# Optimization experiments

Hardware: AMD Instinct MI355X
Metric: run time of the kernel (lower is better)

The kernel has to match this reference:

```python
import jax, jax.numpy as jnp
import numpy as np

N, E, IN_DIM, H, D = 50000, 800000, 256, 4, 128
ALPHA = 0.2  # TF leaky_relu default


def setup_inputs() -> dict:
    key = jax.random.key(0)
    ks = jax.random.split(key, 8)
    s = 0.05  # glorot-like small init to keep exp() stable
    return {
        'features': jax.random.normal(ks[0], (N, IN_DIM), jnp.float32),
        'adj_indices': jax.random.randint(ks[1], (E, 2), 0, N, dtype=jnp.int64),
        'adj_values': jax.random.uniform(ks[2], (E,), jnp.float32),
        'W_trans': jax.random.normal(ks[3], (H, IN_DIM, D), jnp.float32) * s,
        'w_ftx': jax.random.normal(ks[4], (H, D, 1), jnp.float32) * s,
        'w_fty': jax.random.normal(ks[5], (H, D, 1), jnp.float32) * s,
        'w_view': jax.random.normal(ks[6], (H, 2 * D, 1), jnp.float32) * s,
        'bias': jnp.zeros((H, D), jnp.float32),
    }


def _seg_softmax(vals, seg, n):
    # tf.sparse_softmax: softmax over the explicit entries of each row
    m = jax.ops.segment_max(vals, seg, num_segments=n)
    m = jnp.where(jnp.isfinite(m), m, 0.0)  # rows with no edges
    e = jnp.exp(vals - m[seg])
    s = jax.ops.segment_sum(e, seg, num_segments=n)
    return e / s[seg]


def _forward(features, adj_indices, adj_values, W_trans, w_ftx, w_fty, w_view, bias):
    src = adj_indices[:, 0]
    dst = adj_indices[:, 1]
    n = features.shape[0]
    heads = []
    for h in range(W_trans.shape[0]):  # small fixed head count
        ft = features @ W_trans[h]  # [N, D]
        # tf.nn.l2_normalize(axis=1)
        ftn = ft * jax.lax.rsqrt(jnp.maximum(jnp.sum(ft * ft, axis=1, keepdims=True), 1e-12))
        # sim view: cosine similarity on edges
        sim_vals = jnp.sum(ftn[src] * ftn[dst], axis=1)  # [E]
        # nn view: GAT-style logits, leaky_relu, sparse softmax over rows
        ftx = (ft @ w_ftx[h])[:, 0]  # [N]
        fty = (ft @ w_fty[h])[:, 0]  # [N]
        nn_vals = _seg_softmax(jax.nn.leaky_relu(ftx[src] + fty[dst], ALPHA), src, n)
        # view representations: self + (click, sim, nn) each re-softmaxed then aggregated
        view_reprs = [ft]
        for vals in (adj_values, sim_vals, nn_vals):
            p = _seg_softmax(vals, src, n)  # [E]
            view_reprs.append(jax.ops.segment_sum(p[:, None] * ft[dst], src, num_segments=n))
        # learned view mixing: leaky_relu(concat(ft, repr) @ w_view), softmax(exp(.))
        va = [jax.nn.leaky_relu((jnp.concatenate([ft, vr], axis=1) @ w_view[h])[:, 0], ALPHA)
              for vr in view_reprs]
        coefs = jax.nn.softmax(jnp.exp(jnp.stack(va, axis=1)), axis=1)  # [N, 4]
        out = sum(vr * coefs[:, i:i + 1] for i, vr in enumerate(view_reprs)) + bias[h]
        heads.append(jax.nn.elu(out))
    return jnp.concatenate(heads, axis=-1)  # [N, H*D]


def reference(features, adj_indices, adj_values, W_trans, w_ftx, w_fty, w_view, bias):
    return _forward(features, adj_indices, adj_values, W_trans, w_ftx, w_fty, w_view, bias)
```

## Files before the change

kernel.cpp:

```cpp
#include <hip/hip_runtime.h>
#include <math.h>

#define LALPHA 0.2f

using bf16x8 = __attribute__((ext_vector_type(8))) short;
using f32x4 = __attribute__((ext_vector_type(4))) float;
using f32x2 = __attribute__((ext_vector_type(2))) float;

__device__ __forceinline__ float wave_sum(float v) {
#pragma unroll
  for (int off = 32; off > 0; off >>= 1) v += __shfl_xor(v, off);
  return v;
}
__device__ __forceinline__ float grp_sum(float v) {
#pragma unroll
  for (int off = 8; off > 0; off >>= 1) v += __shfl_xor(v, off);
  return v;
}
__device__ __forceinline__ float grp_max(float v) {
#pragma unroll
  for (int off = 8; off > 0; off >>= 1) v = fmaxf(v, __shfl_xor(v, off));
  return v;
}
__device__ __forceinline__ float lrelu(float x) { return x >= 0.f ? x : LALPHA * x; }

__device__ __forceinline__ f32x2 bfp2(unsigned int u) {
  f32x2 r;
  r[0] = __uint_as_float(u << 16);
  r[1] = __uint_as_float(u & 0xffff0000u);
  return r;
}
__device__ __forceinline__ unsigned short f2bf(float x) {
  unsigned int b = __float_as_uint(x);
  return (unsigned short)((b + 0x7fffu + ((b >> 16) & 1u)) >> 16);
}
__device__ __forceinline__ unsigned int cvtpk(float lo, float hi) {
  unsigned int r;
  asm("v_cvt_pk_bf16_f32 %0, %1, %2" : "=v"(r) : "v"(lo), "v"(hi));
  return r;
}

__global__ void hist_kernel(const int* __restrict__ adj, int* __restrict__ deg, int E) {
  for (int e = blockIdx.x * blockDim.x + threadIdx.x; e < E; e += gridDim.x * blockDim.x)
    atomicAdd(&deg[adj[2 * e]], 1);
}

__global__ __launch_bounds__(1024) void scan_a(const int* __restrict__ deg,
                                               int* __restrict__ row_ptr,
                                               int* __restrict__ tilesum, int n) {
  __shared__ int sm[1024];
  int tid = threadIdx.x;
  int idx = blockIdx.x * 1024 + tid;
  int v = (idx < n) ? deg[idx] : 0;
  sm[tid] = v;
  __syncthreads();
  for (int off = 1; off < 1024; off <<= 1) {
    int t = (tid >= off) ? sm[tid - off] : 0;
    __syncthreads();
    sm[tid] += t;
    __syncthreads();
  }
  if (idx < n) row_ptr[idx] = sm[tid] - v;
  if (tid == 1023) tilesum[blockIdx.x] = sm[1023];
}

__global__ __launch_bounds__(1024) void scan_b(int* __restrict__ tilesum, int ntiles) {
  __shared__ int sm[1024];
  int tid = threadIdx.x;
  int v = (tid < ntiles) ? tilesum[tid] : 0;
  sm[tid] = v;
  __syncthreads();
  for (int off = 1; off < 1024; off <<= 1) {
    int t = (tid >= off) ? sm[tid - off] : 0;
    __syncthreads();
    sm[tid] += t;
    __syncthreads();
  }
  if (tid < ntiles) tilesum[tid] = sm[tid] - v;
  if (tid == ntiles - 1) tilesum[ntiles] = sm[tid];
}

__global__ __launch_bounds__(1024) void scan_c(int* __restrict__ row_ptr,
                                               const int* __restrict__ tilesum, int n,
                                               int ntiles) {
  int idx = blockIdx.x * 1024 + threadIdx.x;
  if (idx < n) row_ptr[idx] += tilesum[blockIdx.x];
  if (idx == 0) row_ptr[n] = tilesum[ntiles];
}

__global__ void scatter_kernel(const int* __restrict__ adj, const float* __restrict__ av,
                               const int* __restrict__ row_ptr, int* __restrict__ cursor,
                               int2* __restrict__ csr_ew, int E) {
  for (int e = blockIdx.x * blockDim.x + threadIdx.x; e < E; e += gridDim.x * blockDim.x) {
    int s = adj[2 * e], d = adj[2 * e + 1];
    int pos = row_ptr[s] + atomicAdd(&cursor[s], 1);
    csr_ew[pos] = make_int2(d, __float_as_int(av[e]));
  }
}

__global__ void transw_kernel(const float* __restrict__ W, unsigned short* __restrict__ WT) {
  int idx = blockIdx.x * 256 + threadIdx.x;
  int d = idx & 127;
  int k = (idx >> 7) & 255;
  int h = idx >> 15;
  WT[((size_t)h * 128 + d) * 256 + k] = f2bf(W[idx]);
}

__global__ __launch_bounds__(256) void gemm_mfma(
    const float* __restrict__ A, const unsigned short* __restrict__ WT,
    unsigned short* __restrict__ ft, const float* __restrict__ w_ftx,
    const float* __restrict__ w_fty, float* __restrict__ rnorm, float* __restrict__ ftx,
    float* __restrict__ fty, int N, int H) {
  __shared__ unsigned short tile[4][32][136];
  const int K = 256;
  int h = blockIdx.x;
  int w = threadIdx.x >> 6;
  int r0 = blockIdx.y * 128 + w * 32;
  int lane = threadIdx.x & 63;
  int lr = lane & 15, lg = lane >> 4;
  int ra0 = min(r0 + lr, N - 1);
  int ra1 = min(r0 + 16 + lr, N - 1);
  const float* pa0 = A + (size_t)ra0 * K + lg * 8;
  const float* pa1 = A + (size_t)ra1 * K + lg * 8;
  const unsigned short* pb = WT + ((size_t)h * 128 + lr) * K + lg * 8;
  size_t st = (size_t)H * 128;

  f32x4 acc[2][8] = {};
  for (int k0 = 0; k0 < K; k0 += 32) {
    union {
      bf16x8 v;
      unsigned int u[4];
    } a0, a1;
    float4 f0 = *(const float4*)(pa0 + k0);
    float4 f1 = *(const float4*)(pa0 + k0 + 4);
    a0.u[0] = cvtpk(f0.x, f0.y);
    a0.u[1] = cvtpk(f0.z, f0.w);
    a0.u[2] = cvtpk(f1.x, f1.y);
    a0.u[3] = cvtpk(f1.z, f1.w);
    float4 g0 = *(const float4*)(pa1 + k0);
    float4 g1 = *(const float4*)(pa1 + k0 + 4);
    a1.u[0] = cvtpk(g0.x, g0.y);
    a1.u[1] = cvtpk(g0.z, g0.w);
    a1.u[2] = cvtpk(g1.x, g1.y);
    a1.u[3] = cvtpk(g1.z, g1.w);
    bf16x8 b[8];
#pragma unroll
    for (int cb = 0; cb < 8; ++cb) b[cb] = *(const bf16x8*)(pb + (size_t)cb * 16 * K + k0);
#pragma unroll
    for (int cb = 0; cb < 8; ++cb) {
      acc[0][cb] = __builtin_amdgcn_mfma_f32_16x16x32_bf16(a0.v, b[cb], acc[0][cb], 0, 0, 0);
      acc[1][cb] = __builtin_amdgcn_mfma_f32_16x16x32_bf16(a1.v, b[cb], acc[1][cb], 0, 0, 0);
    }
  }
#pragma unroll
  for (int i = 0; i < 2; ++i) {
#pragma unroll
    for (int cb = 0; cb < 8; ++cb) {
      int rbase = i * 16 + lg * 4;
      int col = cb * 16 + lr;
      unsigned int u01 = cvtpk(acc[i][cb][0], acc[i][cb][1]);
      unsigned int u23 = cvtpk(acc[i][cb][2], acc[i][cb][3]);
      tile[w][rbase + 0][col] = (unsigned short)u01;
      tile[w][rbase + 1][col] = (unsigned short)(u01 >> 16);
      tile[w][rbase + 2][col] = (unsigned short)u23;
      tile[w][rbase + 3][col] = (unsigned short)(u23 >> 16);
    }
  }
#pragma unroll
  for (int rr = 0; rr < 8; ++rr) {
    int row = rr * 4 + lg;
    int nb = r0 + row;
    if (nb < N) {
      *(uint4*)&ft[(size_t)nb * st + (size_t)h * 128 + lr * 8] =
          *(const uint4*)&tile[w][row][lr * 8];
    }
  }
  {
    int row = lane >> 1;
    int ch = lane & 1;
    int nb = r0 + row;
    const float* wx = w_ftx + (size_t)h * 128 + ch * 64;
    const float* wy = w_fty + (size_t)h * 128 + ch * 64;
    float ss = 0.f, sx = 0.f, sy = 0.f;
#pragma unroll
    for (int c8 = 0; c8 < 8; ++c8) {
      const unsigned int* tp = (const unsigned int*)&tile[w][row][ch * 64 + c8 * 8];
      f32x2 f0 = bfp2(tp[0]), f1 = bfp2(tp[1]), f2 = bfp2(tp[2]), f3 = bfp2(tp[3]);
      float4 x0 = *(const float4*)(wx + c8 * 8);
      float4 x1 = *(const float4*)(wx + c8 * 8 + 4);
      float4 y0 = *(const float4*)(wy + c8 * 8);
      float4 y1 = *(const float4*)(wy + c8 * 8 + 4);
      ss += f0[0] * f0[0] + f0[1] * f0[1] + f1[0] * f1[0] + f1[1] * f1[1] +
            f2[0] * f2[0] + f2[1] * f2[1] + f3[0] * f3[0] + f3[1] * f3[1];
      sx += f0[0] * x0.x + f0[1] * x0.y + f1[0] * x0.z + f1[1] * x0.w + f2[0] * x1.x +
            f2[1] * x1.y + f3[0] * x1.z + f3[1] * x1.w;
      sy += f0[0] * y0.x + f0[1] * y0.y + f1[0] * y0.z + f1[1] * y0.w + f2[0] * y1.x +
            f2[1] * y1.y + f3[0] * y1.z + f3[1] * y1.w;
    }
    ss += __shfl_xor(ss, 1);
    sx += __shfl_xor(sx, 1);
    sy += __shfl_xor(sy, 1);
    if (ch == 0 && nb < N) {
      rnorm[(size_t)nb * 4 + h] = rsqrtf(fmaxf(ss, 1e-12f));
      ftx[(size_t)nb * 4 + h] = sx;
      fty[(size_t)nb * 4 + h] = sy;
    }
  }
}

__global__ __launch_bounds__(256) void aggregate_kernel(
    const unsigned short* __restrict__ ft, const float* __restrict__ ftx,
    const float* __restrict__ fty, const float* __restrict__ rnorm,
    const int* __restrict__ row_ptr, const int2* __restrict__ csr_ew,
    const float* __restrict__ w_view, const float* __restrict__ bias,
    float* __restrict__ out, int N, int H) {
  __shared__ float4 wbuf[4][64][4];
  __shared__ int dbuf[4][64];
  int wslot = threadIdx.x >> 6;
  int n = blockIdx.x * 4 + wslot;
  int lane = threadIdx.x & 63;
  int lg = lane >> 4, ll = lane & 15;
  if (n >= N) return;
  int start = __builtin_amdgcn_readfirstlane(row_ptr[n]);
  int end = __builtin_amdgcn_readfirstlane(row_ptr[n + 1]);
  int deg = end - start;
  const uint4* ft4 = (const uint4*)ft;
  float ftx_nh = ftx[(size_t)n * 4 + lg];
  float rn_n = rnorm[(size_t)n * 4 + lg];

  uint4 su = ft4[(size_t)n * 64 + lane];
  f32x2 fsu[4] = {bfp2(su.x), bfp2(su.y), bfp2(su.z), bfp2(su.w)};

  auto dot_own = [&](uint4 u) -> float {
    f32x2 pp = bfp2(u.x) * fsu[0];
    pp += bfp2(u.y) * fsu[1];
    pp += bfp2(u.z) * fsu[2];
    pp += bfp2(u.w) * fsu[3];
    return grp_sum(pp[0] + pp[1]);
  };

  f32x2 Oa[4] = {}, Os[4] = {}, On[4] = {};
  float ss = 0.f;

  auto process = [&](uint4 u, float4 wv) {
    float d = dot_own(u);
    float es = __expf(d * rn_n * wv.z);
    ss += es;
    f32x2 f[4] = {bfp2(u.x), bfp2(u.y), bfp2(u.z), bfp2(u.w)};
#pragma unroll
    for (int k = 0; k < 4; ++k) {
      Oa[k] += f[k] * wv.x;
      Os[k] += f[k] * es;
      On[k] += f[k] * wv.y;
    }
  };

  if (deg > 0 && deg <= 64) {
    float wc[4], vc[4], rnd[4];
    int dc[4];
    float mxn = -INFINITY;
#pragma unroll
    for (int t = 0; t < 4; ++t) {
      int idx = t * 16 + ll;
      bool in = idx < deg;
      int j = in ? (start + idx) : start;
      int2 ew = csr_ew[j];
      wc[t] = in ? __int_as_float(ew.y) : -INFINITY;
      dc[t] = ew.x;
      rnd[t] = rnorm[(size_t)dc[t] * 4 + lg];
      vc[t] = in ? lrelu(ftx_nh + fty[(size_t)dc[t] * 4 + lg]) : -INFINITY;
      mxn = fmaxf(mxn, vc[t]);
    }
    mxn = grp_max(mxn);
    float ea[4], e1[4];
    float sa = 0.f, s1 = 0.f;
#pragma unroll
    for (int t = 0; t < 4; ++t) {
      ea[t] = __expf(wc[t] - 1.f);
      e1[t] = __expf(vc[t] - mxn);
      sa += ea[t];
      s1 += e1[t];
    }
    sa = grp_sum(sa);
    float inv1 = 1.f / grp_sum(s1);
    float en[4];
    float s2 = 0.f;
#pragma unroll
    for (int t = 0; t < 4; ++t) {
      bool in = (t * 16 + ll) < deg;
      en[t] = in ? __expf((e1[t] - 1.f) * inv1) : 0.f;
      s2 += en[t];
    }
    s2 = grp_sum(s2);
    float ra = 1.f / sa, rn2 = 1.f / s2;
#pragma unroll
    for (int t = 0; t < 4; ++t) {
      int idx = t * 16 + ll;
      if (idx < deg) {
        wbuf[wslot][idx][lg] = make_float4(ea[t] * ra, en[t] * rn2, rnd[t], 0.f);
        if (lg == 0) dbuf[wslot][idx] = dc[t] * 64;
      }
    }
    int jj = 0;
    for (; jj + 8 <= deg; jj += 8) {
      int r[8];
      float4 wv[8];
      uint4 u[8];
#pragma unroll
      for (int t = 0; t < 8; ++t) r[t] = dbuf[wslot][jj + t];
#pragma unroll
      for (int t = 0; t < 8; ++t) wv[t] = wbuf[wslot][jj + t][lg];
#pragma unroll
      for (int t = 0; t < 8; ++t) u[t] = ft4[r[t] + lane];
#pragma unroll
      for (int t = 0; t < 8; ++t) process(u[t], wv[t]);
    }
    for (; jj + 4 <= deg; jj += 4) {
      int r0 = dbuf[wslot][jj + 0], r1 = dbuf[wslot][jj + 1];
      int r2 = dbuf[wslot][jj + 2], r3 = dbuf[wslot][jj + 3];
      float4 w0 = wbuf[wslot][jj + 0][lg], w1 = wbuf[wslot][jj + 1][lg];
      float4 w2 = wbuf[wslot][jj + 2][lg], w3 = wbuf[wslot][jj + 3][lg];
      uint4 u0 = ft4[r0 + lane], u1 = ft4[r1 + lane];
      uint4 u2 = ft4[r2 + lane], u3 = ft4[r3 + lane];
      process(u0, w0);
      process(u1, w1);
      process(u2, w2);
      process(u3, w3);
    }
    for (; jj < deg; ++jj) {
      int r0 = dbuf[wslot][jj];
      float4 w0 = wbuf[wslot][jj][lg];
      uint4 u0 = ft4[r0 + lane];
      process(u0, w0);
    }
  } else if (deg > 0) {
    float mxn = -INFINITY;
    for (int idx = ll; idx < deg; idx += 16) {
      int j = start + idx;
      mxn = fmaxf(mxn, lrelu(ftx_nh + fty[(size_t)csr_ew[j].x * 4 + lg]));
    }
    mxn = grp_max(mxn);
    float sa = 0.f, s1 = 0.f;
    for (int idx = ll; idx < deg; idx += 16) {
      int j = start + idx;
      int2 ew = csr_ew[j];
      sa += __expf(__int_as_float(ew.y) - 1.f);
      s1 += __expf(lrelu(ftx_nh + fty[(size_t)ew.x * 4 + lg]) - mxn);
    }
    sa = grp_sum(sa);
    float inv1 = 1.f / grp_sum(s1);
    float s2 = 0.f;
    for (int idx = ll; idx < deg; idx += 16) {
      int j = start + idx;
      float e1 = __expf(lrelu(ftx_nh + fty[(size_t)csr_ew[j].x * 4 + lg]) - mxn);
      s2 += __expf((e1 - 1.f) * inv1);
    }
    s2 = grp_sum(s2);
    float ra = 1.f / sa, rn2 = 1.f / s2;
    for (int c0 = 0; c0 < deg; c0 += 64) {
      int cnt = min(64, deg - c0);
#pragma unroll
      for (int t = 0; t < 4; ++t) {
        int loc = t * 16 + ll;
        if (loc < cnt) {
          int j = start + c0 + loc;
          int2 ew = csr_ew[j];
          int d = ew.x;
          float pa = __expf(__int_as_float(ew.y) - 1.f) * ra;
          float e1 = __expf(lrelu(ftx_nh + fty[(size_t)d * 4 + lg]) - mxn);
          float pn = __expf((e1 - 1.f) * inv1) * rn2;
          wbuf[wslot][loc][lg] = make_float4(pa, pn, rnorm[(size_t)d * 4 + lg], 0.f);
          if (lg == 0) dbuf[wslot][loc] = d * 64;
        }
      }
      for (int jj = 0; jj < cnt; ++jj) {
        int r0 = dbuf[wslot][jj];
        float4 w0 = wbuf[wslot][jj][lg];
        uint4 u0 = ft4[r0 + lane];
        process(u0, w0);
      }
    }
  }

  if (deg > 0) {
    float rs = 1.f / ss;
#pragma unroll
    for (int k = 0; k < 4; ++k) Os[k] *= rs;
  }

  f32x2* fi = fsu;
  const float4* wa4 = (const float4*)&w_view[(size_t)lg * 256 + ll * 8];
  const float4* wb4 = (const float4*)&w_view[(size_t)lg * 256 + 128 + ll * 8];
  float4 wa0 = wa4[0], wa1 = wa4[1];
  float4 wb0 = wb4[0], wb1 = wb4[1];
  float waf[8] = {wa0.x, wa0.y, wa0.z, wa0.w, wa1.x, wa1.y, wa1.z, wa1.w};
  float wbf[8] = {wb0.x, wb0.y, wb0.z, wb0.w, wb1.x, wb1.y, wb1.z, wb1.w};
  float d0 = 0.f, b0 = 0.f, b1 = 0.f, b2 = 0.f, b3 = 0.f;
#pragma unroll
  for (int k = 0; k < 4; ++k) {
    d0 += fi[k][0] * waf[2 * k] + fi[k][1] * waf[2 * k + 1];
    b0 += fi[k][0] * wbf[2 * k] + fi[k][1] * wbf[2 * k + 1];
    b1 += Oa[k][0] * wbf[2 * k] + Oa[k][1] * wbf[2 * k + 1];
    b2 += Os[k][0] * wbf[2 * k] + Os[k][1] * wbf[2 * k + 1];
    b3 += On[k][0] * wbf[2 * k] + On[k][1] * wbf[2 * k + 1];
  }
  d0 = grp_sum(d0);
  b0 = grp_sum(b0);
  b1 = grp_sum(b1);
  b2 = grp_sum(b2);
  b3 = grp_sum(b3);
  float z0 = __expf(lrelu(d0 + b0));
  float z1 = __expf(lrelu(d0 + b1));
  float z2 = __expf(lrelu(d0 + b2));
  float z3 = __expf(lrelu(d0 + b3));
  float zm = fmaxf(fmaxf(z0, z1), fmaxf(z2, z3));
  float c0 = __expf(z0 - zm), c1 = __expf(z1 - zm), c2 = __expf(z2 - zm),
        c3 = __expf(z3 - zm);
  float rcs = 1.f / (c0 + c1 + c2 + c3);
  c0 *= rcs;
  c1 *= rcs;
  c2 *= rcs;
  c3 *= rcs;
  const float4* bb4 = (const float4*)&bias[(size_t)lg * 128 + ll * 8];
  float4 bv0 = bb4[0], bv1 = bb4[1];
  float bbf[8] = {bv0.x, bv0.y, bv0.z, bv0.w, bv1.x, bv1.y, bv1.z, bv1.w};
  float of[8];
#pragma unroll
  for (int k = 0; k < 4; ++k) {
    float ox = c0 * fi[k][0] + c1 * Oa[k][0] + c2 * Os[k][0] + c3 * On[k][0] + bbf[2 * k];
    float oy =
        c0 * fi[k][1] + c1 * Oa[k][1] + c2 * Os[k][1] + c3 * On[k][1] + bbf[2 * k + 1];
    of[2 * k] = ox > 0.f ? ox : expm1f(ox);
    of[2 * k + 1] = oy > 0.f ? oy : expm1f(oy);
  }
  float4* po = (float4*)&out[(size_t)n * 512 + lane * 8];
  po[0] = make_float4(of[0], of[1], of[2], of[3]);
  po[1] = make_float4(of[4], of[5], of[6], of[7]);
}

extern "C" void kernel_launch(void* const* d_in, const int* in_sizes, int n_in,
                              void* d_out, int out_size, void* d_ws, size_t ws_size,
                              hipStream_t stream) {
  const float* features = (const float*)d_in[0];
  const int* adj = (const int*)d_in[1];
  const float* adj_val = (const float*)d_in[2];
  const float* W_trans = (const float*)d_in[3];
  const float* w_ftx = (const float*)d_in[4];
  const float* w_fty = (const float*)d_in[5];
  const float* w_view = (const float*)d_in[6];
  const float* bias = (const float*)d_in[7];
  float* out = (float*)d_out;

  const int IN_DIM = 256, D = 128;
  const int N = in_sizes[0] / IN_DIM;
  const int E = in_sizes[2];
  const int H = in_sizes[7] / D;

  char* p = (char*)d_ws;
  auto alloc = [&](size_t bytes) {
    char* r = p;
    p += (bytes + 255) & ~(size_t)255;
    return r;
  };
  unsigned short* ft = (unsigned short*)alloc((size_t)N * H * D * 2);
  float* rnorm = (float*)alloc((size_t)N * H * 4);
  float* ftx = (float*)alloc((size_t)N * H * 4);
  float* fty = (float*)alloc((size_t)N * H * 4);
  int* row_ptr = (int*)alloc((size_t)(N + 1) * 4);
  int* deg = (int*)alloc((size_t)N * 4);
  int* cursor = (int*)alloc((size_t)N * 4);
  int2* csr_ew = (int2*)alloc((size_t)E * 8);
  unsigned short* WT = (unsigned short*)alloc((size_t)H * IN_DIM * D * 2);
  int* tilesum = (int*)alloc(4096 * 4);
  (void)ws_size;
  (void)n_in;
  (void)out_size;

  int ntiles = (N + 1023) / 1024;

  hipMemsetAsync(deg, 0, (size_t)N * 4, stream);
  hipMemsetAsync(cursor, 0, (size_t)N * 4, stream);
  hist_kernel<<<1024, 256, 0, stream>>>(adj, deg, E);
  scan_a<<<ntiles, 1024, 0, stream>>>(deg, row_ptr, tilesum, N);
  scan_b<<<1, 1024, 0, stream>>>(tilesum, ntiles);
  scan_c<<<ntiles, 1024, 0, stream>>>(row_ptr, tilesum, N, ntiles);
  scatter_kernel<<<1024, 256, 0, stream>>>(adj, adj_val, row_ptr, cursor, csr_ew, E);

  transw_kernel<<<(H * IN_DIM * D) / 256, 256, 0, stream>>>(W_trans, WT);
  dim3 ggrid(H, (N + 127) / 128);
  gemm_mfma<<<ggrid, 256, 0, stream>>>(features, WT, ft, w_ftx, w_fty, rnorm, ftx, fty, N,
                                       H);

  dim3 agrid((N + 3) / 4);
  aggregate_kernel<<<agrid, 256, 0, stream>>>(ft, ftx, fty, rnorm, row_ptr, csr_ew, w_view,
                                              bias, out, N, H);
}
```

Baseline: 346.3 us.

## Share bf16 A tile across heads in GEMM and pack fty with rnorm

The GEMM now gives each block 32 rows with one wave per head. The block loads and converts the fp32 feature rows to bf16 once into shared memory, so features are no longer read and converted four times, once per head. Separately, fty and rnorm are packed into one float2 array, so the aggregate kernel's per-neighbour gathers fetch both values in a single load. The cost is more shared memory per block, fewer rows per block, and a block-wide sync before the MFMA loop.

```diff
diff --git a/kernel.cpp b/kernel.cpp
--- a/kernel.cpp
+++ b/kernel.cpp
@@ -7,11 +7,6 @@
 using f32x4 = __attribute__((ext_vector_type(4))) float;
 using f32x2 = __attribute__((ext_vector_type(2))) float;
 
-__device__ __forceinline__ float wave_sum(float v) {
-#pragma unroll
-  for (int off = 32; off > 0; off >>= 1) v += __shfl_xor(v, off);
-  return v;
-}
 __device__ __forceinline__ float grp_sum(float v) {
 #pragma unroll
   for (int off = 8; off > 0; off >>= 1) v += __shfl_xor(v, off);
@@ -109,47 +104,44 @@
 __global__ __launch_bounds__(256) void gemm_mfma(
     const float* __restrict__ A, const unsigned short* __restrict__ WT,
     unsigned short* __restrict__ ft, const float* __restrict__ w_ftx,
-    const float* __restrict__ w_fty, float* __restrict__ rnorm, float* __restrict__ ftx,
-    float* __restrict__ fty, int N, int H) {
+    const float* __restrict__ w_fty, float2* __restrict__ nprm, float* __restrict__ ftx,
+    int N, int H) {
+  __shared__ unsigned short As[32][264];
   __shared__ unsigned short tile[4][32][136];
   const int K = 256;
-  int h = blockIdx.x;
-  int w = threadIdx.x >> 6;
-  int r0 = blockIdx.y * 128 + w * 32;
+  int h = threadIdx.x >> 6;
+  int r0 = blockIdx.x * 32;
   int lane = threadIdx.x & 63;
   int lr = lane & 15, lg = lane >> 4;
-  int ra0 = min(r0 + lr, N - 1);
-  int ra1 = min(r0 + 16 + lr, N - 1);
-  const float* pa0 = A + (size_t)ra0 * K + lg * 8;
-  const float* pa1 = A + (size_t)ra1 * K + lg * 8;
+  size_t st = (size_t)H * 128;
+
+  {
+    int arow = threadIdx.x >> 3;
+    int acol = (threadIdx.x & 7) * 32;
+    int ra = min(r0 + arow, N - 1);
+    const float* ap = A + (size_t)ra * K + acol;
+    unsigned short* asp = &As[arow][acol];
+#pragma unroll
+    for (int i = 0; i < 8; ++i) {
+      float4 v = *(const float4*)(ap + i * 4);
+      *(unsigned int*)(asp + i * 4) = cvtpk(v.x, v.y);
+      *(unsigned int*)(asp + i * 4 + 2) = cvtpk(v.z, v.w);
+    }
+  }
+  __syncthreads();
+
   const unsigned short* pb = WT + ((size_t)h * 128 + lr) * K + lg * 8;
-  size_t st = (size_t)H * 128;
-
   f32x4 acc[2][8] = {};
   for (int k0 = 0; k0 < K; k0 += 32) {
-    union {
-      bf16x8 v;
-      unsigned int u[4];
-    } a0, a1;
-    float4 f0 = *(const float4*)(pa0 + k0);
-    float4 f1 = *(const float4*)(pa0 + k0 + 4);
-    a0.u[0] = cvtpk(f0.x, f0.y);
-    a0.u[1] = cvtpk(f0.z, f0.w);
-    a0.u[2] = cvtpk(f1.x, f1.y);
-    a0.u[3] = cvtpk(f1.z, f1.w);
-    float4 g0 = *(const float4*)(pa1 + k0);
-    float4 g1 = *(const float4*)(pa1 + k0 + 4);
-    a1.u[0] = cvtpk(g0.x, g0.y);
-    a1.u[1] = cvtpk(g0.z, g0.w);
-    a1.u[2] = cvtpk(g1.x, g1.y);
-    a1.u[3] = cvtpk(g1.z, g1.w);
+    bf16x8 a0 = *(const bf16x8*)&As[lr][k0 + lg * 8];
+    bf16x8 a1 = *(const bf16x8*)&As[16 + lr][k0 + lg * 8];
     bf16x8 b[8];
 #pragma unroll
     for (int cb = 0; cb < 8; ++cb) b[cb] = *(const bf16x8*)(pb + (size_t)cb * 16 * K + k0);
 #pragma unroll
     for (int cb = 0; cb < 8; ++cb) {
-      acc[0][cb] = __builtin_amdgcn_mfma_f32_16x16x32_bf16(a0.v, b[cb], acc[0][cb], 0, 0, 0);
-      acc[1][cb] = __builtin_amdgcn_mfma_f32_16x16x32_bf16(a1.v, b[cb], acc[1][cb], 0, 0, 0);
+      acc[0][cb] = __builtin_amdgcn_mfma_f32_16x16x32_bf16(a0, b[cb], acc[0][cb], 0, 0, 0);
+      acc[1][cb] = __builtin_amdgcn_mfma_f32_16x16x32_bf16(a1, b[cb], acc[1][cb], 0, 0, 0);
     }
   }
 #pragma unroll
@@ -160,10 +152,10 @@
       int col = cb * 16 + lr;
       unsigned int u01 = cvtpk(acc[i][cb][0], acc[i][cb][1]);
       unsigned int u23 = cvtpk(acc[i][cb][2], acc[i][cb][3]);
-      tile[w][rbase + 0][col] = (unsigned short)u01;
-      tile[w][rbase + 1][col] = (unsigned short)(u01 >> 16);
-      tile[w][rbase + 2][col] = (unsigned short)u23;
-      tile[w][rbase + 3][col] = (unsigned short)(u23 >> 16);
+      tile[h][rbase + 0][col] = (unsigned short)u01;
+      tile[h][rbase + 1][col] = (unsigned short)(u01 >> 16);
+      tile[h][rbase + 2][col] = (unsigned short)u23;
+      tile[h][rbase + 3][col] = (unsigned short)(u23 >> 16);
     }
   }
 #pragma unroll
@@ -172,7 +164,7 @@
     int nb = r0 + row;
     if (nb < N) {
       *(uint4*)&ft[(size_t)nb * st + (size_t)h * 128 + lr * 8] =
-          *(const uint4*)&tile[w][row][lr * 8];
+          *(const uint4*)&tile[h][row][lr * 8];
     }
   }
   {
@@ -184,7 +176,7 @@
     float ss = 0.f, sx = 0.f, sy = 0.f;
 #pragma unroll
     for (int c8 = 0; c8 < 8; ++c8) {
-      const unsigned int* tp = (const unsigned int*)&tile[w][row][ch * 64 + c8 * 8];
+      const unsigned int* tp = (const unsigned int*)&tile[h][row][ch * 64 + c8 * 8];
       f32x2 f0 = bfp2(tp[0]), f1 = bfp2(tp[1]), f2 = bfp2(tp[2]), f3 = bfp2(tp[3]);
       float4 x0 = *(const float4*)(wx + c8 * 8);
       float4 x1 = *(const float4*)(wx + c8 * 8 + 4);
@@ -201,19 +193,17 @@
     sx += __shfl_xor(sx, 1);
     sy += __shfl_xor(sy, 1);
     if (ch == 0 && nb < N) {
-      rnorm[(size_t)nb * 4 + h] = rsqrtf(fmaxf(ss, 1e-12f));
+      nprm[(size_t)nb * 4 + h] = make_float2(sy, rsqrtf(fmaxf(ss, 1e-12f)));
       ftx[(size_t)nb * 4 + h] = sx;
-      fty[(size_t)nb * 4 + h] = sy;
     }
   }
 }
 
 __global__ __launch_bounds__(256) void aggregate_kernel(
     const unsigned short* __restrict__ ft, const float* __restrict__ ftx,
-    const float* __restrict__ fty, const float* __restrict__ rnorm,
-    const int* __restrict__ row_ptr, const int2* __restrict__ csr_ew,
-    const float* __restrict__ w_view, const float* __restrict__ bias,
-    float* __restrict__ out, int N, int H) {
+    const float2* __restrict__ nprm, const int* __restrict__ row_ptr,
+    const int2* __restrict__ csr_ew, const float* __restrict__ w_view,
+    const float* __restrict__ bias, float* __restrict__ out, int N, int H) {
   __shared__ float4 wbuf[4][64][4];
   __shared__ int dbuf[4][64];
   int wslot = threadIdx.x >> 6;
@@ -226,7 +216,7 @@
   int deg = end - start;
   const uint4* ft4 = (const uint4*)ft;
   float ftx_nh = ftx[(size_t)n * 4 + lg];
-  float rn_n = rnorm[(size_t)n * 4 + lg];
+  float rn_n = nprm[(size_t)n * 4 + lg].y;
 
   uint4 su = ft4[(size_t)n * 64 + lane];
   f32x2 fsu[4] = {bfp2(su.x), bfp2(su.y), bfp2(su.z), bfp2(su.w)};
@@ -267,8 +257,9 @@
       int2 ew = csr_ew[j];
       wc[t] = in ? __int_as_float(ew.y) : -INFINITY;
       dc[t] = ew.x;
-      rnd[t] = rnorm[(size_t)dc[t] * 4 + lg];
-      vc[t] = in ? lrelu(ftx_nh + fty[(size_t)dc[t] * 4 + lg]) : -INFINITY;
+      float2 pr = nprm[(size_t)dc[t] * 4 + lg];
+      rnd[t] = pr.y;
+      vc[t] = in ? lrelu(ftx_nh + pr.x) : -INFINITY;
       mxn = fmaxf(mxn, vc[t]);
     }
     mxn = grp_max(mxn);
@@ -337,7 +328,7 @@
     float mxn = -INFINITY;
     for (int idx = ll; idx < deg; idx += 16) {
       int j = start + idx;
-      mxn = fmaxf(mxn, lrelu(ftx_nh + fty[(size_t)csr_ew[j].x * 4 + lg]));
+      mxn = fmaxf(mxn, lrelu(ftx_nh + nprm[(size_t)csr_ew[j].x * 4 + lg].x));
     }
     mxn = grp_max(mxn);
     float sa = 0.f, s1 = 0.f;
@@ -345,14 +336,14 @@
       int j = start + idx;
       int2 ew = csr_ew[j];
       sa += __expf(__int_as_float(ew.y) - 1.f);
-      s1 += __expf(lrelu(ftx_nh + fty[(size_t)ew.x * 4 + lg]) - mxn);
+      s1 += __expf(lrelu(ftx_nh + nprm[(size_t)ew.x * 4 + lg].x) - mxn);
     }
     sa = grp_sum(sa);
     float inv1 = 1.f / grp_sum(s1);
     float s2 = 0.f;
     for (int idx = ll; idx < deg; idx += 16) {
       int j = start + idx;
-      float e1 = __expf(lrelu(ftx_nh + fty[(size_t)csr_ew[j].x * 4 + lg]) - mxn);
+      float e1 = __expf(lrelu(ftx_nh + nprm[(size_t)csr_ew[j].x * 4 + lg].x) - mxn);
       s2 += __expf((e1 - 1.f) * inv1);
     }
     s2 = grp_sum(s2);
@@ -366,10 +357,11 @@
           int j = start + c0 + loc;
           int2 ew = csr_ew[j];
           int d = ew.x;
+          float2 pr = nprm[(size_t)d * 4 + lg];
           float pa = __expf(__int_as_float(ew.y) - 1.f) * ra;
-          float e1 = __expf(lrelu(ftx_nh + fty[(size_t)d * 4 + lg]) - mxn);
+          float e1 = __expf(lrelu(ftx_nh + pr.x) - mxn);
           float pn = __expf((e1 - 1.f) * inv1) * rn2;
-          wbuf[wslot][loc][lg] = make_float4(pa, pn, rnorm[(size_t)d * 4 + lg], 0.f);
+          wbuf[wslot][loc][lg] = make_float4(pa, pn, pr.y, 0.f);
           if (lg == 0) dbuf[wslot][loc] = d * 64;
         }
       }
@@ -463,9 +455,8 @@
     return r;
   };
   unsigned short* ft = (unsigned short*)alloc((size_t)N * H * D * 2);
-  float* rnorm = (float*)alloc((size_t)N * H * 4);
+  float2* nprm = (float2*)alloc((size_t)N * H * 8);
   float* ftx = (float*)alloc((size_t)N * H * 4);
-  float* fty = (float*)alloc((size_t)N * H * 4);
   int* row_ptr = (int*)alloc((size_t)(N + 1) * 4);
   int* deg = (int*)alloc((size_t)N * 4);
   int* cursor = (int*)alloc((size_t)N * 4);
@@ -487,11 +478,10 @@
   scatter_kernel<<<1024, 256, 0, stream>>>(adj, adj_val, row_ptr, cursor, csr_ew, E);
 
   transw_kernel<<<(H * IN_DIM * D) / 256, 256, 0, stream>>>(W_trans, WT);
-  dim3 ggrid(H, (N + 127) / 128);
-  gemm_mfma<<<ggrid, 256, 0, stream>>>(features, WT, ft, w_ftx, w_fty, rnorm, ftx, fty, N,
-                                       H);
+  gemm_mfma<<<(N + 31) / 32, 256, 0, stream>>>(features, WT, ft, w_ftx, w_fty, nprm, ftx,
+                                               N, H);
 
   dim3 agrid((N + 3) / 4);
-  aggregate_kernel<<<agrid, 256, 0, stream>>>(ft, ftx, fty, rnorm, row_ptr, csr_ew, w_view,
-                                              bias, out, N, H);
-}
+  aggregate_kernel<<<agrid, 256, 0, stream>>>(ft, ftx, nprm, row_ptr, csr_ew, w_view, bias,
+                                              out, N, H);
+}
```

Measured after the change: 338.7 us. 1.02x faster.
